# Performance work log

Measured on AMD Instinct MI355X. Metric: run time of the kernel, lower is better.

## Reference

```python
import jax, jax.numpy as jnp
import numpy as np

N, D, F, M, K = 4096, 1024, 4096, 2048, 307
EPS = 1e-5

def _ln(h, g, b):
    mu = jnp.mean(h, axis=-1, keepdims=True)
    var = jnp.mean(jnp.square(h - mu), axis=-1, keepdims=True)
    return (h - mu) * jax.lax.rsqrt(var + EPS) * g + b

def _attn(h, wq, wk, wv, mask):
    # wq/wk/wv stored as [D, D] so y = h @ w matches torch Linear(h) with W.T
    q = h @ wq
    k = h @ wk
    v = h @ wv
    s = (q @ k.T) * (1.0 / np.sqrt(D))  # [N, N]
    s = jnp.where(mask, -1e9, s)
    a = jax.nn.softmax(s, axis=-1)
    return a @ v, a

def _ffn(h, w1, b1, w2, b2):
    return jax.nn.gelu(h @ w1 + b1, approximate=False) @ w2 + b2

def setup_inputs() -> dict:
    ks = jax.random.split(jax.random.key(0), 32)
    s = 0.02
    p = lambda i, shape: (jax.random.normal(ks[i], shape, jnp.float32) * s)
    inp = {
        'x': jax.random.normal(ks[0], (N, D), jnp.float32),
        'real_edge_mask': jax.random.bernoulli(ks[1], 0.5, (N, N)),
        'fake_edge_mask': jax.random.bernoulli(ks[2], 0.5, (N, N)),
        'mask_nodes': jax.random.permutation(ks[3], N)[:M].astype(jnp.int32),
        'gene_idx': jnp.argsort(jax.random.uniform(ks[4], (M, D)), axis=-1)[:, :K].astype(jnp.int32),
        'wq1': p(5, (D, D)), 'wk1': p(6, (D, D)), 'wv1': p(7, (D, D)),
        'g1': jnp.ones((D,)), 'be1': jnp.zeros((D,)),
        'fw1': p(8, (D, F)), 'fb1': jnp.zeros((F,)),
        'fw2': p(9, (F, D)), 'fb2': jnp.zeros((D,)),
        'g2': jnp.ones((D,)), 'be2': jnp.zeros((D,)),
        'wq2': p(10, (D, D)), 'wk2': p(11, (D, D)), 'wv2': p(12, (D, D)),
        'g3': jnp.ones((D,)), 'be3': jnp.zeros((D,)),
        'hw1': p(13, (D, F)), 'hb1': jnp.zeros((F,)),
        'hw2': p(14, (F, D)), 'hb2': jnp.zeros((D,)),
        'g4': jnp.ones((D,)), 'be4': jnp.zeros((D,)),
        'head_w': p(15, (D, D)), 'head_b': jnp.zeros((D,)),
    }
    return inp

def reference(x, real_edge_mask, fake_edge_mask, mask_nodes, gene_idx,
              wq1, wk1, wv1, g1, be1, fw1, fb1, fw2, fb2, g2, be2,
              wq2, wk2, wv2, g3, be3, hw1, hb1, hw2, hb2, g4, be4,
              head_w, head_b):
    rows = jnp.arange(M)[:, None]  # [M, 1]
    # encoding_mask_nodes: zero K genes in each of M masked cells
    mask_x = x[mask_nodes].at[rows, gene_idx].set(0.0)
    use_x = x.at[mask_nodes].set(mask_x)

    hidden, encode_weights = _attn(use_x, wq1, wk1, wv1, real_edge_mask)
    hidden = _ln(hidden + use_x, g1, be1)
    hidden = _ln(hidden + _ffn(hidden, fw1, fb1, fw2, fb2), g2, be2)
    # NOTE: original `hidden[mask_nodes][gene_mask] = 0` is a no-op (copy), reproduced.

    recon, _decode_weights = _attn(hidden, wq2, wk2, wv2, real_edge_mask)
    recon = _ln(recon + hidden, g3, be3)
    recon = _ln(recon + _ffn(recon, hw1, hb1, hw2, hb2), g4, be4)
    h = recon @ head_w + head_b

    x_init = x[mask_nodes][rows, gene_idx]   # [M, K]
    x_recon = h[mask_nodes][rows, gene_idx]  # [M, K]
    return x_init, x_recon, encode_weights, recon
```

## Files before the change

kernel.cpp:

```cpp
#include <hip/hip_runtime.h>
#include <math.h>
#include <stdint.h>

typedef unsigned short u16;
typedef __attribute__((ext_vector_type(8))) short bf16x8;
typedef __attribute__((ext_vector_type(4))) float f32x4;

#define N_ 4096
#define D_ 1024
#define F_ 4096
#define M_ 2048
#define KG 307

__device__ __forceinline__ u16 f2bf(float f) {
  unsigned int u = __float_as_uint(f);
  unsigned int r = u + 0x7fffu + ((u >> 16) & 1u);
  return (u16)(r >> 16);
}

__device__ __forceinline__ void gl_lds16(const u16* g, u16* l) {
  __builtin_amdgcn_global_load_lds(
      (__attribute__((address_space(1))) void*)(void*)g,
      (__attribute__((address_space(3))) void*)(void*)l,
      16, 0, 0);
}

enum { E_QKV = 0, E_SMASK = 1, E_PART = 2, E_GELU = 3 };
#define SMEM_BYTES 131072

template <int EPI>
__global__ __launch_bounds__(512, 2) void gemm256(
    const u16* __restrict__ A, const u16* __restrict__ B,
    void* __restrict__ C, void* __restrict__ C2,
    int gridM, int gridN, int Ndim, int Ksp, int lda, int ldb, long zstr,
    const float* __restrict__ bias, const unsigned char* __restrict__ mask,
    float scale) {
  extern __shared__ __align__(16) char smem[];
  const int tid = threadIdx.x;
  const int lane = tid & 63;
  const int wid = tid >> 6;
  const int wr = wid >> 2;
  const int wc = wid & 3;
  const int lr = lane & 15;
  const int lk = lane >> 4;

  {
  }
  const int nwg = gridM * gridN;
  const int bid = blockIdx.x;
  const int q8 = nwg >> 3, r8 = nwg & 7;
  const int xcd = bid & 7, ii = bid >> 3;
  int wg = (xcd < r8 ? xcd * (q8 + 1) : r8 * (q8 + 1) + (xcd - r8) * q8) + ii;
  const int rowblk = wg / (gridN << 2);
  const int rem = wg - rowblk * (gridN << 2);
  const int mrem = gridM - (rowblk << 2);
  int mtile, ntile;
  if (mrem >= 4) {
    ntile = rem >> 2;
    mtile = (rowblk << 2) + (rem & 3);
  } else {
    ntile = rem / mrem;
    mtile = (rowblk << 2) + (rem - ntile * mrem);
  }
  const long bm = (long)mtile * 256;
  const long bn = (long)ntile * 256;
  const long koff = (long)blockIdx.y * Ksp;

  auto stage = [&](int s, int t) {
    const long k0 = koff + (long)t * 32;
    u16* base = (u16*)(smem + s * 32768);
#pragma unroll
    for (int j = 0; j < 2; ++j) {
      int o = (j << 9) + tid;
      int row = o >> 2;
      int scb = ((o & 3) << 4) ^ (((row >> 1) & 3) << 4);
      gl_lds16(A + (bm + row) * (long)lda + k0 + (scb >> 1), base + o * 8);
    }
    u16* baseB = base + 8192;
#pragma unroll
    for (int j = 0; j < 2; ++j) {
      int o = (j << 9) + tid;
      int row = o >> 2;
      int scb = ((o & 3) << 4) ^ (((row >> 1) & 3) << 4);
      gl_lds16(B + (bn + row) * (long)ldb + k0 + (scb >> 1), baseB + o * 8);
    }
  };

  stage(0, 0);
  __builtin_amdgcn_sched_barrier(0);
  stage(1, 1);
  __builtin_amdgcn_sched_barrier(0);
  stage(2, 2);
  __builtin_amdgcn_sched_barrier(0);

  f32x4 acc[8][4];
#pragma unroll
  for (int m = 0; m < 8; ++m)
#pragma unroll
    for (int n = 0; n < 4; ++n) acc[m][n] = f32x4{0.f, 0.f, 0.f, 0.f};

  const int NT = Ksp >> 5;
  for (int t = 0; t < NT; ++t) {
    const int s = t & 3;
    const int left = NT - 1 - t;
    if (left >= 2)
      asm volatile("s_waitcnt vmcnt(8)" ::: "memory");
    else if (left == 1)
      asm volatile("s_waitcnt vmcnt(4)" ::: "memory");
    else
      asm volatile("s_waitcnt vmcnt(0)" ::: "memory");
    __builtin_amdgcn_s_barrier();
    __builtin_amdgcn_sched_barrier(0);

    const char* baseA = smem + s * 32768;
    const char* baseB = baseA + 16384;
    bf16x8 av[8], bv[4];
#pragma unroll
    for (int n = 0; n < 4; ++n) {
      int row = (wc << 6) + (n << 4) + lr;
      int cb = (lk << 4) ^ (((row >> 1) & 3) << 4);
      bv[n] = *(const bf16x8*)(baseB + row * 64 + cb);
    }
#pragma unroll
    for (int m = 0; m < 8; ++m) {
      int row = (wr << 7) + (m << 4) + lr;
      int cb = (lk << 4) ^ (((row >> 1) & 3) << 4);
      av[m] = *(const bf16x8*)(baseA + row * 64 + cb);
    }
    if (t + 3 < NT) stage((t + 3) & 3, t + 3);

    __builtin_amdgcn_s_setprio(1);
#pragma unroll
    for (int m = 0; m < 8; ++m)
#pragma unroll
      for (int n = 0; n < 4; ++n)
        acc[m][n] = __builtin_amdgcn_mfma_f32_16x16x32_bf16(av[m], bv[n], acc[m][n], 0, 0, 0);
    __builtin_amdgcn_s_setprio(0);
  }

  const bool z0 = (blockIdx.y == 0);
  float* Cz = (float*)C + (long)blockIdx.y * zstr;
#pragma unroll
  for (int m = 0; m < 8; ++m) {
#pragma unroll
    for (int n = 0; n < 4; ++n) {
#pragma unroll
      for (int j = 0; j < 4; ++j) {
        long row = bm + (wr << 7) + (m << 4) + (lk << 2) + j;
        long col = bn + (wc << 6) + (n << 4) + lr;
        float v = acc[m][n][j];
        if constexpr (EPI == E_QKV) {
          if (col < 2048)
            ((u16*)C)[row * 2048 + col] = f2bf(v);
          else
            ((u16*)C2)[(col - 2048) * (long)N_ + row] = f2bf(v);
        } else if constexpr (EPI == E_SMASK) {
          v *= scale;
          if (mask[row * Ndim + col]) v = -1e9f;
          ((float*)C)[row * Ndim + col] = v;
        } else if constexpr (EPI == E_PART) {
          Cz[row * Ndim + col] = v + ((z0 && bias) ? bias[col] : 0.f);
        } else if constexpr (EPI == E_GELU) {
          float tv = v + bias[col];
          float gl = 0.5f * tv * (1.0f + erff(tv * 0.70710678118654752f));
          ((u16*)C)[row * Ndim + col] = f2bf(gl);
        }
      }
    }
  }
}

__global__ __launch_bounds__(256) void gemm_nt_bias(
    const u16* __restrict__ A, const u16* __restrict__ B, float* __restrict__ C,
    int Ndim, int K, int lda, int ldb, const float* __restrict__ bias) {
  __shared__ u16 As[2][128 * 32];
  __shared__ u16 Bs[2][128 * 32];
  const int tid = threadIdx.x;
  const int lane = tid & 63;
  const int wid = tid >> 6;
  const int wr = wid >> 1;
  const int wc = wid & 1;
  const int lr = lane & 15;
  const int lk = lane >> 4;
  const long bm = (long)blockIdx.x * 128;
  const long bn = (long)blockIdx.y * 128;

  f32x4 acc[4][4];
#pragma unroll
  for (int i = 0; i < 4; ++i)
#pragma unroll
    for (int j = 0; j < 4; ++j) acc[i][j] = f32x4{0.f, 0.f, 0.f, 0.f};

  auto stage = [&](int buf, long k0) {
#pragma unroll
    for (int i = 0; i < 2; ++i) {
      int c = tid + i * 256;
      gl_lds16(A + (bm + (c >> 2)) * (long)lda + k0 + (c & 3) * 8, As[buf] + c * 8);
    }
#pragma unroll
    for (int i = 0; i < 2; ++i) {
      int c = tid + i * 256;
      gl_lds16(B + (bn + (c >> 2)) * (long)ldb + k0 + (c & 3) * 8, Bs[buf] + c * 8);
    }
  };

  stage(0, 0);
  __syncthreads();
  const int nt = K / 32;
  int cur = 0;
  for (int t = 0; t < nt; ++t) {
    if (t + 1 < nt) stage(cur ^ 1, (long)(t + 1) * 32);
    bf16x8 av[4], bv[4];
#pragma unroll
    for (int mr = 0; mr < 4; ++mr)
      av[mr] = *(const bf16x8*)(As[cur] + (wr * 64 + mr * 16 + lr) * 32 + lk * 8);
#pragma unroll
    for (int nr = 0; nr < 4; ++nr)
      bv[nr] = *(const bf16x8*)(Bs[cur] + (wc * 64 + nr * 16 + lr) * 32 + lk * 8);
#pragma unroll
    for (int mr = 0; mr < 4; ++mr)
#pragma unroll
      for (int nr = 0; nr < 4; ++nr)
        acc[mr][nr] = __builtin_amdgcn_mfma_f32_16x16x32_bf16(av[mr], bv[nr], acc[mr][nr], 0, 0, 0);
    __syncthreads();
    cur ^= 1;
  }
#pragma unroll
  for (int mr = 0; mr < 4; ++mr)
#pragma unroll
    for (int nr = 0; nr < 4; ++nr)
#pragma unroll
      for (int j = 0; j < 4; ++j) {
        long row = bm + wr * 64 + mr * 16 + lk * 4 + j;
        long col = bn + wc * 64 + nr * 16 + lr;
        C[row * Ndim + col] = acc[mr][nr][j] + bias[col];
      }
}

__global__ __launch_bounds__(256) void tcvt(const float* __restrict__ in,
                                            u16* __restrict__ out, int R, int C) {
  __shared__ float tile[32][33];
  int bx = blockIdx.x * 32;
  int by = blockIdx.y * 32;
  int tx = threadIdx.x & 31;
  int ty = threadIdx.x >> 5;
#pragma unroll
  for (int i = 0; i < 32; i += 8)
    tile[ty + i][tx] = in[(long)(by + ty + i) * C + bx + tx];
  __syncthreads();
#pragma unroll
  for (int i = 0; i < 32; i += 8)
    out[(long)(bx + ty + i) * R + by + tx] = f2bf(tile[tx][ty + i]);
}

__global__ void copy_usex(const float* __restrict__ x, float* __restrict__ xf,
                          u16* __restrict__ xb, long n) {
  long i = (long)blockIdx.x * blockDim.x + threadIdx.x;
  if (i < n) {
    float v = x[i];
    xf[i] = v;
    xb[i] = f2bf(v);
  }
}

__global__ void mask_zero(const float* __restrict__ x, const int* __restrict__ mask_nodes,
                          const int* __restrict__ gene_idx, float* __restrict__ xf,
                          u16* __restrict__ xb, float* __restrict__ x_init) {
  int m = blockIdx.x;
  int k = threadIdx.x;
  if (k >= KG) return;
  int row = mask_nodes[m];
  int col = gene_idx[m * KG + k];
  x_init[m * KG + k] = x[(long)row * D_ + col];
  xf[(long)row * D_ + col] = 0.f;
  xb[(long)row * D_ + col] = 0;
}

template <int NY>
__global__ __launch_bounds__(256) void add_ln(const float* __restrict__ y, long ystr,
                                              const float* __restrict__ r,
                                              const float* __restrict__ g,
                                              const float* __restrict__ b,
                                              float* __restrict__ of, u16* __restrict__ ob) {
  int row = blockIdx.x;
  const float* yr = y + (long)row * D_;
  const float* rr = r + (long)row * D_;
  float v[4];
  float s = 0.f, ss = 0.f;
#pragma unroll
  for (int i = 0; i < 4; ++i) {
    int idx = threadIdx.x + i * 256;
    float t = rr[idx];
#pragma unroll
    for (int z = 0; z < NY; ++z) t += yr[z * ystr + idx];
    v[i] = t;
    s += t;
    ss += t * t;
  }
#pragma unroll
  for (int o = 32; o > 0; o >>= 1) {
    s += __shfl_down(s, o, 64);
    ss += __shfl_down(ss, o, 64);
  }
  __shared__ float red[8];
  int wid = threadIdx.x >> 6, lane = threadIdx.x & 63;
  if (lane == 0) {
    red[wid] = s;
    red[4 + wid] = ss;
  }
  __syncthreads();
  if (threadIdx.x == 0) {
    red[0] = red[0] + red[1] + red[2] + red[3];
    red[4] = red[4] + red[5] + red[6] + red[7];
  }
  __syncthreads();
  float mu = red[0] * (1.f / D_);
  float var = red[4] * (1.f / D_) - mu * mu;
  float rs = rsqrtf(var + 1e-5f);
#pragma unroll
  for (int i = 0; i < 4; ++i) {
    int idx = threadIdx.x + i * 256;
    float o = (v[i] - mu) * rs * g[idx] + b[idx];
    of[(long)row * D_ + idx] = o;
    ob[(long)row * D_ + idx] = f2bf(o);
  }
}

template <bool WF32>
__global__ __launch_bounds__(256) void softmax_row(const float* __restrict__ sin,
                                                   float* __restrict__ a32,
                                                   u16* __restrict__ a16) {
  int row = blockIdx.x;
  const float* sr = sin + (long)row * N_;
  float v[16];
  float mx = -3.0e38f;
#pragma unroll
  for (int i = 0; i < 16; ++i) {
    v[i] = sr[threadIdx.x + i * 256];
    mx = fmaxf(mx, v[i]);
  }
#pragma unroll
  for (int o = 32; o > 0; o >>= 1) mx = fmaxf(mx, __shfl_down(mx, o, 64));
  __shared__ float red[8];
  int wid = threadIdx.x >> 6, lane = threadIdx.x & 63;
  if (lane == 0) red[wid] = mx;
  __syncthreads();
  if (threadIdx.x == 0) red[0] = fmaxf(fmaxf(red[0], red[1]), fmaxf(red[2], red[3]));
  __syncthreads();
  mx = red[0];
  float sum = 0.f;
#pragma unroll
  for (int i = 0; i < 16; ++i) {
    v[i] = __expf(v[i] - mx);
    sum += v[i];
  }
#pragma unroll
  for (int o = 32; o > 0; o >>= 1) sum += __shfl_down(sum, o, 64);
  if (lane == 0) red[4 + wid] = sum;
  __syncthreads();
  if (threadIdx.x == 0) red[4] = red[4] + red[5] + red[6] + red[7];
  __syncthreads();
  float inv = 1.f / red[4];
#pragma unroll
  for (int i = 0; i < 16; ++i) {
    float p = v[i] * inv;
    long off = (long)row * N_ + threadIdx.x + i * 256;
    if constexpr (WF32) a32[off] = p;
    a16[off] = f2bf(p);
  }
}

__global__ void gather_rows(const u16* __restrict__ src, const int* __restrict__ mask_nodes,
                            u16* __restrict__ dst) {
  int m = blockIdx.x;
  int row = mask_nodes[m];
  for (int i = threadIdx.x; i < D_; i += 256)
    dst[(long)m * D_ + i] = src[(long)row * D_ + i];
}

__global__ void gather_recon(const float* __restrict__ h, const int* __restrict__ gene_idx,
                             float* __restrict__ xr) {
  int m = blockIdx.x;
  int k = threadIdx.x;
  if (k >= KG) return;
  xr[m * KG + k] = h[(long)m * D_ + gene_idx[m * KG + k]];
}

extern "C" void kernel_launch(void* const* d_in, const int* in_sizes, int n_in,
                              void* d_out, int out_size, void* d_ws, size_t ws_size,
                              hipStream_t stream) {
  const float* x = (const float*)d_in[0];
  const unsigned char* real_mask = (const unsigned char*)d_in[1];
  const int* mask_nodes = (const int*)d_in[3];
  const int* gene_idx = (const int*)d_in[4];
  const float* wq1 = (const float*)d_in[5];
  const float* wk1 = (const float*)d_in[6];
  const float* wv1 = (const float*)d_in[7];
  const float* g1 = (const float*)d_in[8];
  const float* be1 = (const float*)d_in[9];
  const float* fw1 = (const float*)d_in[10];
  const float* fb1 = (const float*)d_in[11];
  const float* fw2 = (const float*)d_in[12];
  const float* fb2 = (const float*)d_in[13];
  const float* g2 = (const float*)d_in[14];
  const float* be2 = (const float*)d_in[15];
  const float* wq2 = (const float*)d_in[16];
  const float* wk2 = (const float*)d_in[17];
  const float* wv2 = (const float*)d_in[18];
  const float* g3 = (const float*)d_in[19];
  const float* be3 = (const float*)d_in[20];
  const float* hw1 = (const float*)d_in[21];
  const float* hb1 = (const float*)d_in[22];
  const float* hw2 = (const float*)d_in[23];
  const float* hb2 = (const float*)d_in[24];
  const float* g4 = (const float*)d_in[25];
  const float* be4 = (const float*)d_in[26];
  const float* head_w = (const float*)d_in[27];
  const float* head_b = (const float*)d_in[28];

  float* out_xinit = (float*)d_out;
  float* out_xrecon = out_xinit + (long)M_ * KG;
  float* out_enc = out_xrecon + (long)M_ * KG;
  float* out_recon = out_enc + (long)N_ * N_;

  hipFuncSetAttribute((const void*)gemm256<E_QKV>, hipFuncAttributeMaxDynamicSharedMemorySize, SMEM_BYTES);
  hipFuncSetAttribute((const void*)gemm256<E_SMASK>, hipFuncAttributeMaxDynamicSharedMemorySize, SMEM_BYTES);
  hipFuncSetAttribute((const void*)gemm256<E_PART>, hipFuncAttributeMaxDynamicSharedMemorySize, SMEM_BYTES);
  hipFuncSetAttribute((const void*)gemm256<E_GELU>, hipFuncAttributeMaxDynamicSharedMemorySize, SMEM_BYTES);

  char* w = (char*)d_ws;
  size_t off = 0;
  auto alloc = [&](size_t bytes) {
    void* p = w + off;
    off += (bytes + 255) & ~(size_t)255;
    return p;
  };
  float* useXf = (float*)alloc((size_t)N_ * D_ * 4);
  u16* useXb = (u16*)alloc((size_t)N_ * D_ * 2);
  u16* wslot = (u16*)alloc((size_t)D_ * F_ * 2);
  u16* qkb = (u16*)alloc((size_t)N_ * 2048 * 2);
  u16* vT = (u16*)alloc((size_t)D_ * N_ * 2);
  float* sbuf = (float*)alloc((size_t)N_ * N_ * 4);
  u16* aB = (u16*)alloc((size_t)N_ * N_ * 2);
  float* gout4 = (float*)alloc((size_t)4 * N_ * D_ * 4);
  float* actA = (float*)alloc((size_t)N_ * D_ * 4);
  float* actB = (float*)alloc((size_t)N_ * D_ * 4);
  u16* actB16 = (u16*)alloc((size_t)N_ * D_ * 2);
  u16* tbuf = (u16*)sbuf;
  u16* AgB = qkb;

  const float scale = 1.0f / 32.0f;
  const long nd = (long)N_ * D_;
  dim3 blk(256), blk5(512);

  copy_usex<<<dim3((unsigned)((nd + 255) / 256)), blk, 0, stream>>>(x, useXf, useXb, nd);
  mask_zero<<<dim3(M_), 320, 0, stream>>>(x, mask_nodes, gene_idx, useXf, useXb, out_xinit);

#define TCVT(src, R, C, dst) tcvt<<<dim3((C) / 32, (R) / 32), blk, 0, stream>>>(src, dst, R, C)
#define G256(EP, GM, GN, Z, A, B, C, C2, ND, KS, LA, LB, ZS, BI, MK, SC)                        \
  gemm256<EP><<<dim3((GM) * (GN), Z), blk5, SMEM_BYTES, stream>>>(A, B, C, C2, GM, GN, ND, KS, \
                                                                  LA, LB, ZS, BI, MK, SC)

  TCVT(wq1, D_, D_, wslot);
  TCVT(wk1, D_, D_, wslot + 1024 * 1024);
  TCVT(wv1, D_, D_, wslot + 2048 * 1024);
  G256(E_QKV, 16, 12, 1, useXb, wslot, qkb, vT, 3072, 1024, 1024, 1024, 0, nullptr, nullptr, 0.f);
  G256(E_SMASK, 16, 16, 1, qkb, qkb + 1024, out_enc, nullptr, 4096, 1024, 2048, 2048, 0, nullptr, real_mask, scale);
  softmax_row<true><<<dim3(N_), blk, 0, stream>>>(out_enc, out_enc, aB);
  G256(E_PART, 16, 4, 4, aB, vT, gout4, nullptr, 1024, 1024, 4096, 4096, nd, nullptr, nullptr, 0.f);
  add_ln<4><<<dim3(N_), blk, 0, stream>>>(gout4, nd, useXf, g1, be1, actA, actB16);
  TCVT(fw1, D_, F_, wslot);
  G256(E_GELU, 16, 16, 1, actB16, wslot, tbuf, nullptr, 4096, 1024, 1024, 1024, 0, fb1, nullptr, 0.f);
  TCVT(fw2, F_, D_, wslot);
  G256(E_PART, 16, 4, 4, tbuf, wslot, gout4, nullptr, 1024, 1024, 4096, 4096, nd, fb2, nullptr, 0.f);
  add_ln<4><<<dim3(N_), blk, 0, stream>>>(gout4, nd, actA, g2, be2, actB, actB16);

  TCVT(wq2, D_, D_, wslot);
  TCVT(wk2, D_, D_, wslot + 1024 * 1024);
  TCVT(wv2, D_, D_, wslot + 2048 * 1024);
  G256(E_QKV, 16, 12, 1, actB16, wslot, qkb, vT, 3072, 1024, 1024, 1024, 0, nullptr, nullptr, 0.f);
  G256(E_SMASK, 16, 16, 1, qkb, qkb + 1024, sbuf, nullptr, 4096, 1024, 2048, 2048, 0, nullptr, real_mask, scale);
  softmax_row<false><<<dim3(N_), blk, 0, stream>>>(sbuf, nullptr, aB);
  G256(E_PART, 16, 4, 4, aB, vT, gout4, nullptr, 1024, 1024, 4096, 4096, nd, nullptr, nullptr, 0.f);
  add_ln<4><<<dim3(N_), blk, 0, stream>>>(gout4, nd, actB, g3, be3, actA, actB16);
  TCVT(hw1, D_, F_, wslot);
  G256(E_GELU, 16, 16, 1, actB16, wslot, tbuf, nullptr, 4096, 1024, 1024, 1024, 0, hb1, nullptr, 0.f);
  TCVT(hw2, F_, D_, wslot);
  G256(E_PART, 16, 4, 4, tbuf, wslot, gout4, nullptr, 1024, 1024, 4096, 4096, nd, hb2, nullptr, 0.f);
  add_ln<4><<<dim3(N_), blk, 0, stream>>>(gout4, nd, actA, g4, be4, out_recon, actB16);

  gather_rows<<<dim3(M_), blk, 0, stream>>>(actB16, mask_nodes, AgB);
  TCVT(head_w, D_, D_, wslot);
  gemm_nt_bias<<<dim3(16, 8), blk, 0, stream>>>(AgB, wslot, gout4, 1024, 1024, 1024, 1024, head_b);
  gather_recon<<<dim3(M_), 320, 0, stream>>>(gout4, gene_idx, out_xrecon);
#undef TCVT
#undef G256
}
```

Baseline: 702.7 us.

## Restructure GEMM main loop to 64-wide K tiles with staggered A/B prefetch

The GEMM main loop now uses 64-element K tiles instead of 32 and keeps separate double-buffered LDS regions for A and B. B is prefetched two iterations ahead and A one ahead. Each K tile is split into four quarter phases separated by barriers, and each phase issues one half-tile global-to-LDS load while it runs MFMAs on that quarter's rows. The aim is to halve barrier and waitcnt overhead per K and spread load issue across the compute. In exchange there are extra intra-iteration barriers, a new XOR swizzle for 128-byte rows, and a requirement that Ksp be a multiple of 64.

Result: no change. 703.2 us (+0.1%).

```diff
diff --git a/kernel.cpp b/kernel.cpp
--- a/kernel.cpp
+++ b/kernel.cpp
@@ -44,8 +44,6 @@
   const int lr = lane & 15;
   const int lk = lane >> 4;
 
-  {
-  }
   const int nwg = gridM * gridN;
   const int bid = blockIdx.x;
   const int q8 = nwg >> 3, r8 = nwg & 7;
@@ -65,33 +63,40 @@
   const long bm = (long)mtile * 256;
   const long bn = (long)ntile * 256;
   const long koff = (long)blockIdx.y * Ksp;
-
-  auto stage = [&](int s, int t) {
-    const long k0 = koff + (long)t * 32;
-    u16* base = (u16*)(smem + s * 32768);
+  const int NT = Ksp >> 6;
+
+  auto stA = [&](int t, int h) {
+    char* base = smem + ((t & 1) << 15) + (h << 14);
+    const long k0 = koff + ((long)t << 6);
 #pragma unroll
     for (int j = 0; j < 2; ++j) {
-      int o = (j << 9) + tid;
-      int row = o >> 2;
-      int scb = ((o & 3) << 4) ^ (((row >> 1) & 3) << 4);
-      gl_lds16(A + (bm + row) * (long)lda + k0 + (scb >> 1), base + o * 8);
-    }
-    u16* baseB = base + 8192;
-#pragma unroll
-    for (int j = 0; j < 2; ++j) {
-      int o = (j << 9) + tid;
-      int row = o >> 2;
-      int scb = ((o & 3) << 4) ^ (((row >> 1) & 3) << 4);
-      gl_lds16(B + (bn + row) * (long)ldb + k0 + (scb >> 1), baseB + o * 8);
+      int o = tid + (j << 9);
+      int r = o >> 3, s = o & 7;
+      gl_lds16(A + (bm + (h << 7) + r) * (long)lda + k0 + ((s ^ (r & 7)) << 3),
+               (u16*)(base + o * 16));
     }
   };
-
-  stage(0, 0);
+  auto stB = [&](int t, int h) {
+    char* base = smem + 65536 + ((t & 1) << 15) + (h << 14);
+    const long k0 = koff + ((long)t << 6);
+#pragma unroll
+    for (int j = 0; j < 2; ++j) {
+      int o = tid + (j << 9);
+      int r = o >> 3, s = o & 7;
+      gl_lds16(B + (bn + (h << 7) + r) * (long)ldb + k0 + ((s ^ (r & 7)) << 3),
+               (u16*)(base + o * 16));
+    }
+  };
+
+  stA(0, 0);
+  stA(0, 1);
+  stB(0, 0);
+  stB(0, 1);
+  if (NT > 1) {
+    stB(1, 0);
+    stB(1, 1);
+  }
   __builtin_amdgcn_sched_barrier(0);
-  stage(1, 1);
-  __builtin_amdgcn_sched_barrier(0);
-  stage(2, 2);
-  __builtin_amdgcn_sched_barrier(0);
 
   f32x4 acc[8][4];
 #pragma unroll
@@ -99,43 +104,62 @@
 #pragma unroll
     for (int n = 0; n < 4; ++n) acc[m][n] = f32x4{0.f, 0.f, 0.f, 0.f};
 
-  const int NT = Ksp >> 5;
   for (int t = 0; t < NT; ++t) {
-    const int s = t & 3;
-    const int left = NT - 1 - t;
-    if (left >= 2)
-      asm volatile("s_waitcnt vmcnt(8)" ::: "memory");
-    else if (left == 1)
+    if (t + 1 < NT)
       asm volatile("s_waitcnt vmcnt(4)" ::: "memory");
     else
       asm volatile("s_waitcnt vmcnt(0)" ::: "memory");
     __builtin_amdgcn_s_barrier();
     __builtin_amdgcn_sched_barrier(0);
 
-    const char* baseA = smem + s * 32768;
-    const char* baseB = baseA + 16384;
-    bf16x8 av[8], bv[4];
-#pragma unroll
-    for (int n = 0; n < 4; ++n) {
-      int row = (wc << 6) + (n << 4) + lr;
-      int cb = (lk << 4) ^ (((row >> 1) & 3) << 4);
-      bv[n] = *(const bf16x8*)(baseB + row * 64 + cb);
+    const char* Ab = smem + ((t & 1) << 15);
+    const char* Bb = smem + 65536 + ((t & 1) << 15);
+    bf16x8 bv[4][2];
+
+#pragma unroll
+    for (int q = 0; q < 4; ++q) {
+      bf16x8 av[2][2];
+#pragma unroll
+      for (int e = 0; e < 2; ++e)
+#pragma unroll
+        for (int ks = 0; ks < 2; ++ks) {
+          int r = (wr << 7) + (q << 5) + (e << 4) + lr;
+          av[e][ks] = *(const bf16x8*)(Ab + r * 128 + ((((ks << 2) | lk) ^ (r & 7)) << 4));
+        }
+      if (q == 0) {
+#pragma unroll
+        for (int n = 0; n < 4; ++n)
+#pragma unroll
+          for (int ks = 0; ks < 2; ++ks) {
+            int r = (wc << 6) + (n << 4) + lr;
+            bv[n][ks] = *(const bf16x8*)(Bb + r * 128 + ((((ks << 2) | lk) ^ (r & 7)) << 4));
+          }
+      }
+      if (q == 0) {
+        if (t + 1 < NT) stA(t + 1, 0);
+      } else if (q == 1) {
+        if (t + 1 < NT) stA(t + 1, 1);
+      } else if (q == 2) {
+        if (t + 2 < NT) stB(t + 2, 0);
+      } else {
+        if (t + 2 < NT) stB(t + 2, 1);
+      }
+
+      __builtin_amdgcn_s_setprio(1);
+#pragma unroll
+      for (int e = 0; e < 2; ++e)
+#pragma unroll
+        for (int n = 0; n < 4; ++n)
+#pragma unroll
+          for (int ks = 0; ks < 2; ++ks)
+            acc[(q << 1) | e][n] =
+                __builtin_amdgcn_mfma_f32_16x16x32_bf16(av[e][ks], bv[n][ks], acc[(q << 1) | e][n], 0, 0, 0);
+      __builtin_amdgcn_s_setprio(0);
+      if (q < 3) {
+        __builtin_amdgcn_s_barrier();
+        __builtin_amdgcn_sched_barrier(0);
+      }
     }
-#pragma unroll
-    for (int m = 0; m < 8; ++m) {
-      int row = (wr << 7) + (m << 4) + lr;
-      int cb = (lk << 4) ^ (((row >> 1) & 3) << 4);
-      av[m] = *(const bf16x8*)(baseA + row * 64 + cb);
-    }
-    if (t + 3 < NT) stage((t + 3) & 3, t + 3);
-
-    __builtin_amdgcn_s_setprio(1);
-#pragma unroll
-    for (int m = 0; m < 8; ++m)
-#pragma unroll
-      for (int n = 0; n < 4; ++n)
-        acc[m][n] = __builtin_amdgcn_mfma_f32_16x16x32_bf16(av[m], bv[n], acc[m][n], 0, 0, 0);
-    __builtin_amdgcn_s_setprio(0);
   }
 
   const bool z0 = (blockIdx.y == 0);
```
